# Kernel tuning notes

Measured on AMD Instinct MI355X. Metric: run time of the kernel, lower is better.

The kernel has to match this reference:

```python
import jax, jax.numpy as jnp
import numpy as np

B = 256      # batch
T = 256      # trajectory_length
V = 1000     # instruction_vocab_size
SD = 64      # state_dim
AD = 64      # action_dim
HD = 256     # hidden_dim
H = HD * 4   # LSTM hidden size = 1024
IN_DIM = HD * 8 + HD * 2 + HD + AD  # 2880 LSTM input size


def setup_inputs() -> dict:
    key = jax.random.key(0)
    ks = jax.random.split(key, 20)
    def rn(k, shape, s=0.02):
        return jax.random.normal(k, shape, dtype=jnp.float32) * s
    z = lambda *s: jnp.zeros(s, jnp.float32)
    return dict(
        start_state=jax.random.normal(ks[0], (B, SD), dtype=jnp.float32),
        instruction_id=jax.random.randint(ks[1], (B,), 0, V),
        emb_W=rn(ks[2], (V, H)),
        enc_W1=rn(ks[3], (H, 2 * H)), enc_b1=z(2 * H),
        enc_W2=rn(ks[4], (2 * H, 2 * H)), enc_b2=z(2 * H),
        s_W1=rn(ks[5], (SD, HD)), s_b1=z(HD),
        s_W2=rn(ks[6], (HD, 2 * HD)), s_b2=z(2 * HD),
        p_W=rn(ks[7], (1, HD)), p_b=z(HD),
        l0_Wih=rn(ks[8], (IN_DIM, 4 * H)), l0_Whh=rn(ks[9], (H, 4 * H)),
        l0_bih=z(4 * H), l0_bhh=z(4 * H),
        l1_Wih=rn(ks[10], (H, 4 * H)), l1_Whh=rn(ks[11], (H, 4 * H)),
        l1_bih=z(4 * H), l1_bhh=z(4 * H),
        e_W=rn(ks[12], (H, H)), e_b=z(H),
        a_W1=rn(ks[13], (H, 2 * HD)), a_b1=z(2 * HD),
        a_W2=rn(ks[14], (2 * HD, AD)), a_b2=z(AD),
        patterns=jax.random.normal(ks[15], (V, T, AD), dtype=jnp.float32) * 0.5,
    )


def _lstm_cell(x, h, c, Wih, Whh, bih, bhh):
    # torch gate order: i, f, g, o
    g = x @ Wih + bih + h @ Whh + bhh
    i, f, gg, o = jnp.split(g, 4, axis=-1)
    c = jax.nn.sigmoid(f) * c + jax.nn.sigmoid(i) * jnp.tanh(gg)
    h = jax.nn.sigmoid(o) * jnp.tanh(c)
    return h, c


def reference(start_state, instruction_id, emb_W, enc_W1, enc_b1, enc_W2, enc_b2,
              s_W1, s_b1, s_W2, s_b2, p_W, p_b,
              l0_Wih, l0_Whh, l0_bih, l0_bhh, l1_Wih, l1_Whh, l1_bih, l1_bhh,
              e_W, e_b, a_W1, a_b1, a_W2, a_b2, patterns):
    bsz = start_state.shape[0]
    traj_len = patterns.shape[1]
    act_dim = patterns.shape[2]
    hid = l0_Whh.shape[0]

    emb = emb_W[instruction_id]                                   # [B, 4h]
    instr_f = jax.nn.relu(emb @ enc_W1 + enc_b1) @ enc_W2 + enc_b2    # [B, 8h]
    start_f = jax.nn.relu(start_state @ s_W1 + s_b1) @ s_W2 + s_b2    # [B, 2h]
    progress = jnp.linspace(0.0, 1.0, traj_len).astype(jnp.float32)   # [T]
    prog_f = jax.nn.relu(progress[:, None] @ p_W + p_b)               # [T, h]

    def step(carry, pf):
        h1, c1, h2, c2, prev = carry
        x = jnp.concatenate(
            [instr_f, start_f, jnp.broadcast_to(pf, (bsz, pf.shape[0])), prev], axis=-1)
        h1, c1 = _lstm_cell(x, h1, c1, l0_Wih, l0_Whh, l0_bih, l0_bhh)
        h2, c2 = _lstm_cell(h1, h2, c2, l1_Wih, l1_Whh, l1_bih, l1_bhh)
        enh = jax.nn.relu(h2 @ e_W + e_b)                             # temporal_enhancer (eval: no dropout)
        act = jax.nn.relu(enh @ a_W1 + a_b1) @ a_W2 + a_b2            # action_predictor
        return (h1, c1, h2, c2, act), act

    zh = jnp.zeros((bsz, hid), jnp.float32)
    a0 = jnp.zeros((bsz, act_dim), jnp.float32)
    _, acts = jax.lax.scan(step, (zh, zh, zh, zh, a0), prog_f)
    predicted_actions = jnp.transpose(acts, (1, 0, 2))                # [B, T, A]
    # NOTE: as in the source, predicted_actions is NOT used by the constraint output.
    del predicted_actions

    # _apply_progressive_constraints
    start_exp = start_state[:, None, :]                               # [B, 1, A]
    w = progress[None, :, None]                                       # [1, T, 1]
    pat = patterns[instruction_id]                                    # [B, T, A]
    target = start_exp + pat
    constrained = start_exp + w * (target - start_exp)
    return constrained
```

## Files before the change

### kernel.cpp

```cpp
#include <hip/hip_runtime.h>

#define BB 256
#define TT 256
#define ADIM 64


typedef unsigned int  u32x4 __attribute__((ext_vector_type(4)));
typedef float         f32x4 __attribute__((ext_vector_type(4)));

static __device__ __forceinline__ float bf_lo(unsigned int u) {
    return __uint_as_float(u << 16);
}
static __device__ __forceinline__ float bf_hi(unsigned int u) {
    return __uint_as_float(u & 0xffff0000u);
}
static __device__ __forceinline__ unsigned short f32_to_bf16_rne(float f) {
    unsigned int x = __float_as_uint(f);
    unsigned int r = x + 0x7fffu + ((x >> 16) & 1u);
    return (unsigned short)(r >> 16);
}
static __device__ __forceinline__ unsigned int pack_bf16(float lo, float hi) {
    return (unsigned int)f32_to_bf16_rne(lo) |
           ((unsigned int)f32_to_bf16_rne(hi) << 16);
}

__global__ __launch_bounds__(256) void traj_kernel(
    const void* __restrict__ start,
    const int*  __restrict__ ids,
    const void* __restrict__ patterns,
    void*       __restrict__ out)
{
    bool isbf;
    {
        const unsigned long long* q = (const unsigned long long*)start;
        unsigned long long d = q[threadIdx.x & 63];
        bool big = false;
#pragma unroll
        for (int i = 0; i < 4; ++i) {
            float v = __uint_as_float(((unsigned int)(unsigned short)(d >> (16 * i))) << 16);
            big |= !(fabsf(v) <= 1.0e4f);
        }
        isbf = (__ballot(big) == 0ull);
    }

    const int tid  = threadIdx.x;
    const int beta = blockIdx.x;
    const int b    = beta >> 2;
    const int t0   = (beta & 3) << 6;
    const int tl   = tid >> 3;
    const int a0   = (tid & 7) << 3;

    const int   t1 = t0 + tl;
    const int   t2 = t1 + 32;
    const float w1 = (float)t1 * (1.0f / 255.0f);
    const float w2 = (float)t2 * (1.0f / 255.0f);

    const int id = ids[b];

    const unsigned soff  = ((unsigned)b << 6) + (unsigned)a0;
    const unsigned loff  = ((unsigned)tl << 6) + (unsigned)a0;
    const unsigned pbase = (unsigned)id * (TT * ADIM) + ((unsigned)t0 << 6) + loff;
    const unsigned obase = (((unsigned)b * TT + (unsigned)t0) << 6) + loff;
    const unsigned step  = 32 * ADIM;

    if (isbf) {
        const unsigned short* s16 = (const unsigned short*)start + soff;
        const unsigned short* p16 = (const unsigned short*)patterns + pbase;
        unsigned short*       o16 = (unsigned short*)out + obase;

        u32x4 sv = *reinterpret_cast<const u32x4*>(s16);
        u32x4 p1 = *reinterpret_cast<const u32x4*>(p16);
        u32x4 p2 = *reinterpret_cast<const u32x4*>(p16 + step);

        u32x4 o1, o2;
#pragma unroll
        for (int i = 0; i < 4; ++i) {
            const float slo = bf_lo(sv[i]);
            const float shi = bf_hi(sv[i]);
            o1[i] = pack_bf16(fmaf(w1, bf_lo(p1[i]), slo),
                              fmaf(w1, bf_hi(p1[i]), shi));
            o2[i] = pack_bf16(fmaf(w2, bf_lo(p2[i]), slo),
                              fmaf(w2, bf_hi(p2[i]), shi));
        }
        __builtin_nontemporal_store(o1, reinterpret_cast<u32x4*>(o16));
        __builtin_nontemporal_store(o2, reinterpret_cast<u32x4*>(o16 + step));
    } else {
        const float* sf = (const float*)start + soff;
        const float* pf = (const float*)patterns + pbase;
        float*       of = (float*)out + obase;

        f32x4 s0 = ((const f32x4*)sf)[0];
        f32x4 s1 = ((const f32x4*)sf)[1];
        f32x4 a0v = ((const f32x4*)pf)[0];
        f32x4 a1v = ((const f32x4*)pf)[1];
        f32x4 b0v = ((const f32x4*)(pf + step))[0];
        f32x4 b1v = ((const f32x4*)(pf + step))[1];

        f32x4 r10, r11, r20, r21;
#pragma unroll
        for (int i = 0; i < 4; ++i) {
            r10[i] = fmaf(w1, a0v[i], s0[i]);
            r11[i] = fmaf(w1, a1v[i], s1[i]);
            r20[i] = fmaf(w2, b0v[i], s0[i]);
            r21[i] = fmaf(w2, b1v[i], s1[i]);
        }
        __builtin_nontemporal_store(r10, (f32x4*)of);
        __builtin_nontemporal_store(r11, (f32x4*)of + 1);
        __builtin_nontemporal_store(r20, (f32x4*)(of + step));
        __builtin_nontemporal_store(r21, (f32x4*)(of + step) + 1);
    }
}

extern "C" void kernel_launch(void* const* d_in, const int* in_sizes, int n_in,
                              void* d_out, int out_size, void* d_ws, size_t ws_size,
                              hipStream_t stream) {
    const void* start = d_in[0];
    const int*  ids   = (const int*)d_in[1];
    int pat_idx = n_in - 1;
    for (int i = 0; i < n_in; ++i) {
        if (in_sizes[i] == 1000 * 256 * 64) { pat_idx = i; break; }
    }
    const void* patterns = d_in[pat_idx];

    traj_kernel<<<1024, 256, 0, stream>>>(start, ids, patterns, d_out);
}
```

Baseline: 9.917 us.

## Use one 1024-thread block per batch row and issue bf16 loads before dtype probe

Changes the grid from 1024 blocks of 256 threads to 256 blocks of 1024 threads, so each block covers a full trajectory for one batch element. It also hoists the bf16 start and pattern loads above the dtype-detection ballot so their memory latency overlaps the probe. The cost is fewer, larger blocks, which can leave CUs unevenly loaded. The speculative bf16 loads also read as bf16 even when inputs are fp32; the fp32 path still reloads its own data.

New measurement: 10.29 us. 1.04x slower.

```diff
diff --git a/kernel.cpp b/kernel.cpp
--- a/kernel.cpp
+++ b/kernel.cpp
@@ -24,16 +24,35 @@
            ((unsigned int)f32_to_bf16_rne(hi) << 16);
 }
 
-__global__ __launch_bounds__(256) void traj_kernel(
+__global__ __launch_bounds__(1024) void traj_kernel(
     const void* __restrict__ start,
     const int*  __restrict__ ids,
     const void* __restrict__ patterns,
     void*       __restrict__ out)
 {
+    const int tid = threadIdx.x;
+    const int b   = blockIdx.x;
+    const int tl  = tid >> 3;
+    const int a0  = (tid & 7) << 3;
+
+    const int id = ids[b];
+
+    const unsigned soff  = ((unsigned)b << 6) + (unsigned)a0;
+    const unsigned loff  = ((unsigned)tl << 6) + (unsigned)a0;
+    const unsigned pbase = (unsigned)id * (TT * ADIM) + loff;
+    const unsigned obase = (((unsigned)b * TT) << 6) + loff;
+    const unsigned step  = 128 * ADIM;
+
+    const unsigned short* s16 = (const unsigned short*)start + soff;
+    const unsigned short* p16 = (const unsigned short*)patterns + pbase;
+    u32x4 sv  = *reinterpret_cast<const u32x4*>(s16);
+    u32x4 pv0 = *reinterpret_cast<const u32x4*>(p16);
+    u32x4 pv1 = *reinterpret_cast<const u32x4*>(p16 + step);
+
     bool isbf;
     {
         const unsigned long long* q = (const unsigned long long*)start;
-        unsigned long long d = q[threadIdx.x & 63];
+        unsigned long long d = q[tid & 63];
         bool big = false;
 #pragma unroll
         for (int i = 0; i < 4; ++i) {
@@ -43,47 +62,21 @@
         isbf = (__ballot(big) == 0ull);
     }
 
-    const int tid  = threadIdx.x;
-    const int beta = blockIdx.x;
-    const int b    = beta >> 2;
-    const int t0   = (beta & 3) << 6;
-    const int tl   = tid >> 3;
-    const int a0   = (tid & 7) << 3;
-
-    const int   t1 = t0 + tl;
-    const int   t2 = t1 + 32;
-    const float w1 = (float)t1 * (1.0f / 255.0f);
-    const float w2 = (float)t2 * (1.0f / 255.0f);
-
-    const int id = ids[b];
-
-    const unsigned soff  = ((unsigned)b << 6) + (unsigned)a0;
-    const unsigned loff  = ((unsigned)tl << 6) + (unsigned)a0;
-    const unsigned pbase = (unsigned)id * (TT * ADIM) + ((unsigned)t0 << 6) + loff;
-    const unsigned obase = (((unsigned)b * TT + (unsigned)t0) << 6) + loff;
-    const unsigned step  = 32 * ADIM;
+    const float w0 = (float)tl         * (1.0f / 255.0f);
+    const float w1 = (float)(tl + 128) * (1.0f / 255.0f);
 
     if (isbf) {
-        const unsigned short* s16 = (const unsigned short*)start + soff;
-        const unsigned short* p16 = (const unsigned short*)patterns + pbase;
-        unsigned short*       o16 = (unsigned short*)out + obase;
-
-        u32x4 sv = *reinterpret_cast<const u32x4*>(s16);
-        u32x4 p1 = *reinterpret_cast<const u32x4*>(p16);
-        u32x4 p2 = *reinterpret_cast<const u32x4*>(p16 + step);
-
-        u32x4 o1, o2;
+        unsigned short* o16 = (unsigned short*)out + obase;
+        u32x4 o0, o1;
 #pragma unroll
         for (int i = 0; i < 4; ++i) {
             const float slo = bf_lo(sv[i]);
             const float shi = bf_hi(sv[i]);
-            o1[i] = pack_bf16(fmaf(w1, bf_lo(p1[i]), slo),
-                              fmaf(w1, bf_hi(p1[i]), shi));
-            o2[i] = pack_bf16(fmaf(w2, bf_lo(p2[i]), slo),
-                              fmaf(w2, bf_hi(p2[i]), shi));
+            o0[i] = pack_bf16(fmaf(w0, bf_lo(pv0[i]), slo), fmaf(w0, bf_hi(pv0[i]), shi));
+            o1[i] = pack_bf16(fmaf(w1, bf_lo(pv1[i]), slo), fmaf(w1, bf_hi(pv1[i]), shi));
         }
-        __builtin_nontemporal_store(o1, reinterpret_cast<u32x4*>(o16));
-        __builtin_nontemporal_store(o2, reinterpret_cast<u32x4*>(o16 + step));
+        __builtin_nontemporal_store(o0, reinterpret_cast<u32x4*>(o16));
+        __builtin_nontemporal_store(o1, reinterpret_cast<u32x4*>(o16 + step));
     } else {
         const float* sf = (const float*)start + soff;
         const float* pf = (const float*)patterns + pbase;
@@ -99,10 +92,10 @@
         f32x4 r10, r11, r20, r21;
 #pragma unroll
         for (int i = 0; i < 4; ++i) {
-            r10[i] = fmaf(w1, a0v[i], s0[i]);
-            r11[i] = fmaf(w1, a1v[i], s1[i]);
-            r20[i] = fmaf(w2, b0v[i], s0[i]);
-            r21[i] = fmaf(w2, b1v[i], s1[i]);
+            r10[i] = fmaf(w0, a0v[i], s0[i]);
+            r11[i] = fmaf(w0, a1v[i], s1[i]);
+            r20[i] = fmaf(w1, b0v[i], s0[i]);
+            r21[i] = fmaf(w1, b1v[i], s1[i]);
         }
         __builtin_nontemporal_store(r10, (f32x4*)of);
         __builtin_nontemporal_store(r11, (f32x4*)of + 1);
@@ -122,5 +115,5 @@
     }
     const void* patterns = d_in[pat_idx];
 
-    traj_kernel<<<1024, 256, 0, stream>>>(start, ids, patterns, d_out);
+    traj_kernel<<<256, 1024, 0, stream>>>(start, ids, patterns, d_out);
 }
```
